# Kernel tuning notes

Hardware: AMD Instinct MI355X
Metric: run time of the kernel (lower is better)

The kernel has to match this reference:

```python
import jax, jax.numpy as jnp
import numpy as np

B, S, DIM = 1, 2048, 2048
H = 16
Q_LORA, KV_LORA = 1536, 512
D_NOPE, D_ROPE, D_V = 128, 64, 128
D_QK = D_NOPE + D_ROPE  # 192
EPS = 1e-6


def rms_norm(x, w, eps=EPS):
    var = jnp.mean(jnp.square(x), axis=-1, keepdims=True)
    return x * jax.lax.rsqrt(var + eps) * w


def apply_rope(x, cos, sin):
    # x: [B,S,H,D] with interleaved complex pairs; cos/sin: [S,D//2]
    x1, x2 = x[..., 0::2], x[..., 1::2]
    c = cos[None, :, None, :]
    s = sin[None, :, None, :]
    o1 = x1 * c - x2 * s
    o2 = x1 * s + x2 * c
    return jnp.stack([o1, o2], axis=-1).reshape(x.shape)


def setup_inputs() -> dict:
    key = jax.random.key(0)
    ks = jax.random.split(key, 8)
    x = jax.random.normal(ks[0], (B, S, DIM), dtype=jnp.float32)
    # rotary tables (standard complex exponentials)
    inv_freq = 1.0 / (10000.0 ** (np.arange(0, D_ROPE, 2, dtype=np.float32) / D_ROPE))
    t = np.arange(S, dtype=np.float32)
    freqs = np.outer(t, inv_freq)  # [S, D_ROPE//2]
    freqs_cos = jnp.asarray(np.cos(freqs))
    freqs_sin = jnp.asarray(np.sin(freqs))
    sd = lambda fan_in: 1.0 / np.sqrt(fan_in)
    wq_a = jax.random.normal(ks[1], (Q_LORA, DIM), dtype=jnp.float32) * sd(DIM)
    q_a_ln_w = jnp.ones((Q_LORA,), dtype=jnp.float32)
    wq_b = jax.random.normal(ks[2], (H * D_QK, Q_LORA), dtype=jnp.float32) * sd(Q_LORA)
    wkv_a = jax.random.normal(ks[3], (KV_LORA + D_ROPE, DIM), dtype=jnp.float32) * sd(DIM)
    kv_a_ln_w = jnp.ones((KV_LORA,), dtype=jnp.float32)
    wkv_b = jax.random.normal(ks[4], (H * (D_NOPE + D_V), KV_LORA), dtype=jnp.float32) * sd(KV_LORA)
    wo = jax.random.normal(ks[5], (DIM, H * D_V), dtype=jnp.float32) * sd(H * D_V)
    return {"x": x, "freqs_cos": freqs_cos, "freqs_sin": freqs_sin,
            "wq_a": wq_a, "q_a_ln_w": q_a_ln_w, "wq_b": wq_b,
            "wkv_a": wkv_a, "kv_a_ln_w": kv_a_ln_w, "wkv_b": wkv_b, "wo": wo}


def reference(x, freqs_cos, freqs_sin, wq_a, q_a_ln_w, wq_b, wkv_a, kv_a_ln_w, wkv_b, wo):
    softmax_scale = D_QK ** -0.5
    # Query: low-rank down-proj -> RMSNorm -> up-proj
    q = rms_norm(x @ wq_a.T, q_a_ln_w) @ wq_b.T            # [B,S,H*D_QK]
    q = q.reshape(B, S, H, D_QK)
    q_nope, q_pe = q[..., :D_NOPE], q[..., D_NOPE:]
    q_pe = apply_rope(q_pe, freqs_cos, freqs_sin)
    # KV: shared low-rank latent + decoupled rope key (MQA-style, 1 head)
    kv = x @ wkv_a.T                                        # [B,S,KV_LORA+D_ROPE]
    kv_c = rms_norm(kv[..., :KV_LORA], kv_a_ln_w)           # [B,S,KV_LORA]
    k_pe = apply_rope(kv[..., None, KV_LORA:], freqs_cos, freqs_sin)  # [B,S,1,D_ROPE]
    kvb = (kv_c @ wkv_b.T).reshape(B, S, H, D_NOPE + D_V)
    k_nope, v = kvb[..., :D_NOPE], kvb[..., D_NOPE:]
    # Attention scores: nope part + shared rope part
    scores = (jnp.einsum('bqhd,bkhd->bhqk', q_nope, k_nope)
              + jnp.einsum('bqhd,bkd->bhqk', q_pe, k_pe[:, :, 0, :])) * softmax_scale
    causal = jnp.tril(jnp.ones((S, S), dtype=bool))
    scores = jnp.where(causal[None, None], scores, -jnp.inf)
    p = jax.nn.softmax(scores, axis=-1)
    out = jnp.einsum('bhqk,bkhd->bqhd', p, v).reshape(B, S, H * D_V)
    return out @ wo.T
```

## Files before the change

### kernel.cpp

```cpp
#include <hip/hip_runtime.h>
#include <cstdint>
#include <cstddef>

typedef __bf16 bf16;
typedef bf16 bf16x8 __attribute__((ext_vector_type(8)));
typedef bf16 bf16x4 __attribute__((ext_vector_type(4)));
typedef float f32x4 __attribute__((ext_vector_type(4)));

typedef __attribute__((address_space(1))) void as1_void;
typedef __attribute__((address_space(3))) void as3_void;

#define INF __builtin_inff()

__global__ __launch_bounds__(256) void z100_cast_all(
    const float* __restrict__ x, const float* __restrict__ wq_a,
    const float* __restrict__ wkv_a, const float* __restrict__ wq_b,
    const float* __restrict__ wkv_b, const float* __restrict__ wo,
    bf16* __restrict__ x_bf, bf16* __restrict__ wab_bf,
    bf16* __restrict__ wqb_bf, bf16* __restrict__ wkvb_bf,
    bf16* __restrict__ wo_bf) {
    int i = blockIdx.x * 256 + threadIdx.x;
    const float* s;
    bf16* d;
    float mul = 1.f;
    if (i < 1048576)      { s = x + (size_t)i * 4;                     d = x_bf + (size_t)i * 4; }
    else if (i < 1835008) { int o = i - 1048576; s = wq_a  + (size_t)o * 4; d = wab_bf + (size_t)o * 4; }
    else if (i < 2129920) { int o = i - 1835008; s = wkv_a + (size_t)o * 4; d = wab_bf + 1536ull * 2048 + (size_t)o * 4; }
    else if (i < 3309568) { int o = i - 2129920; s = wq_b  + (size_t)o * 4; d = wqb_bf + (size_t)o * 4;
                            mul = 0.072168783649f; }
    else if (i < 3833856) { int o = i - 3309568; s = wkv_b + (size_t)o * 4; d = wkvb_bf + (size_t)o * 4; }
    else if (i < 4882432) { int o = i - 3833856; s = wo    + (size_t)o * 4; d = wo_bf + (size_t)o * 4; }
    else {                  int o = i - 4882432; bf16x4 z = {};
                            *(bf16x4*)(wab_bf + 2112ull * 2048 + (size_t)o * 4) = z; return; }
    float4 v = *(const float4*)s;
    bf16x4 ovec = { (bf16)(v.x * mul), (bf16)(v.y * mul), (bf16)(v.z * mul), (bf16)(v.w * mul) };
    *(bf16x4*)d = ovec;
}

__global__ __launch_bounds__(256) void z100_rmsnorm2(
    const bf16* __restrict__ qa, const float* __restrict__ q_ln,
    const float* __restrict__ kv_ln,
    bf16* __restrict__ qan, bf16* __restrict__ kvc) {
    const int bid = blockIdx.x;
    const bf16* xr;
    const float* w;
    bf16* yr;
    int N; float invN;
    if (bid < 2048) { xr = qa + (size_t)bid * 2112;        w = q_ln;  yr = qan + (size_t)bid * 1536; N = 1536; invN = 1.f / 1536.f; }
    else { int r = bid - 2048; xr = qa + (size_t)r * 2112 + 1536; w = kv_ln; yr = kvc + (size_t)r * 512;  N = 512;  invN = 1.f / 512.f; }
    float ss = 0.f;
    for (int i = threadIdx.x * 8; i < N; i += 2048) {
        bf16x8 v = *(const bf16x8*)(xr + i);
        #pragma unroll
        for (int j = 0; j < 8; ++j) { float f = (float)v[j]; ss += f * f; }
    }
    #pragma unroll
    for (int d = 1; d < 64; d <<= 1) ss += __shfl_xor(ss, d);
    __shared__ float red[4];
    if ((threadIdx.x & 63) == 0) red[threadIdx.x >> 6] = ss;
    __syncthreads();
    float tot = red[0] + red[1] + red[2] + red[3];
    float rs = rsqrtf(tot * invN + 1e-6f);
    for (int i = threadIdx.x * 8; i < N; i += 2048) {
        bf16x8 v = *(const bf16x8*)(xr + i);
        float4 w0 = *(const float4*)(w + i);
        float4 w1 = *(const float4*)(w + i + 4);
        bf16x8 o;
        o[0] = (bf16)((float)v[0] * rs * w0.x); o[1] = (bf16)((float)v[1] * rs * w0.y);
        o[2] = (bf16)((float)v[2] * rs * w0.z); o[3] = (bf16)((float)v[3] * rs * w0.w);
        o[4] = (bf16)((float)v[4] * rs * w1.x); o[5] = (bf16)((float)v[5] * rs * w1.y);
        o[6] = (bf16)((float)v[6] * rs * w1.z); o[7] = (bf16)((float)v[7] * rs * w1.w);
        *(bf16x8*)(yr + i) = o;
    }
}

template <typename OutT>
__device__ __forceinline__ void gemm8_body(
    const bf16* __restrict__ A, const bf16* __restrict__ B,
    OutT* __restrict__ C, int N, int K, int ldc, int mblk, int nblk,
    bf16* AsB, bf16* BsB) {
    const int tid = threadIdx.x;
    const int lane = tid & 63, wave = tid >> 6;
    const int l15 = lane & 15, l4 = lane >> 4;
    const int m0 = mblk * 128, n0 = nblk * 128;
    const int wr = (wave >> 1) * 32, wc = (wave & 1) * 64;

    f32x4 acc[2][4] = {};

    const int srow = lane >> 2;
    const int scol = (lane & 3) * 8;
    const size_t a_base = (size_t)(m0 + wave * 16 + srow) * K + scol;
    const size_t b_base = (size_t)(n0 + wave * 16 + srow) * K + scol;

    auto stg = [&](int buf, int k0) {
        __builtin_amdgcn_global_load_lds((as1_void*)(void*)(A + a_base + k0),
                                         (as3_void*)(AsB + buf * 4096 + wave * 512), 16, 0, 0);
        __builtin_amdgcn_global_load_lds((as1_void*)(void*)(B + b_base + k0),
                                         (as3_void*)(BsB + buf * 4096 + wave * 512), 16, 0, 0);
    };

    const int nt = K >> 5;
    stg(0, 0);
    stg(1, 32);
    asm volatile("s_waitcnt vmcnt(2)" ::: "memory");
    __builtin_amdgcn_s_barrier();

    int cb = 0, sb = 2;
    for (int t = 0; t < nt; ++t) {
        if (t + 2 < nt) stg(sb, (t + 2) * 32);
        const bf16* Ab = AsB + cb * 4096;
        const bf16* Bb = BsB + cb * 4096;
        bf16x8 fa[2], fb[4];
        #pragma unroll
        for (int i = 0; i < 2; ++i)
            fa[i] = *(const bf16x8*)(Ab + (wr + 16 * i + l15) * 32 + 8 * l4);
        #pragma unroll
        for (int j = 0; j < 4; ++j)
            fb[j] = *(const bf16x8*)(Bb + (wc + 16 * j + l15) * 32 + 8 * l4);
        #pragma unroll
        for (int i = 0; i < 2; ++i)
            #pragma unroll
            for (int j = 0; j < 4; ++j)
                acc[i][j] = __builtin_amdgcn_mfma_f32_16x16x32_bf16(fa[i], fb[j], acc[i][j], 0, 0, 0);
        if (t + 2 < nt) { asm volatile("s_waitcnt vmcnt(2)" ::: "memory"); }
        else            { asm volatile("s_waitcnt vmcnt(0)" ::: "memory"); }
        __builtin_amdgcn_s_barrier();
        cb = (cb == 2) ? 0 : cb + 1;
        sb = (sb == 2) ? 0 : sb + 1;
    }

    #pragma unroll
    for (int i = 0; i < 2; ++i) {
        int row0 = m0 + wr + 16 * i + 4 * l4;
        #pragma unroll
        for (int j = 0; j < 4; ++j) {
            int col = n0 + wc + 16 * j + l15;
            if (col < N) {
                #pragma unroll
                for (int jj = 0; jj < 4; ++jj)
                    C[(size_t)(row0 + jj) * ldc + col] = (OutT)acc[i][j][jj];
            }
        }
    }
}

__global__ __launch_bounds__(512) void z100_gemm8(
    const bf16* __restrict__ A, const bf16* __restrict__ B,
    float* __restrict__ C, int N, int K, int ldc) {
    __shared__ alignas(16) bf16 As[3 * 128 * 32];
    __shared__ alignas(16) bf16 Bs[3 * 128 * 32];
    gemm8_body<float>(A, B, C, N, K, ldc, blockIdx.y, blockIdx.x, As, Bs);
}

__global__ __launch_bounds__(512) void z100_gemm8_bf(
    const bf16* __restrict__ A, const bf16* __restrict__ B,
    bf16* __restrict__ C, int N, int K, int ldc) {
    __shared__ alignas(16) bf16 As[3 * 128 * 32];
    __shared__ alignas(16) bf16 Bs[3 * 128 * 32];
    gemm8_body<bf16>(A, B, C, N, K, ldc, blockIdx.y, blockIdx.x, As, Bs);
}

__global__ __launch_bounds__(512) void z100_gemm_qkv(
    const bf16* __restrict__ qan, const bf16* __restrict__ wqb, bf16* __restrict__ qf,
    const bf16* __restrict__ kvc, const bf16* __restrict__ wkvb, bf16* __restrict__ kvbf) {
    __shared__ alignas(16) bf16 As[3 * 128 * 32];
    __shared__ alignas(16) bf16 Bs[3 * 128 * 32];
    const int bid = blockIdx.x;
    if (bid < 384) gemm8_body<bf16>(qan, wqb, qf, 3072, 1536, 3072, bid / 24, bid % 24, As, Bs);
    else { int b = bid - 384; gemm8_body<bf16>(kvc, wkvb, kvbf, 4096, 512, 4096, b / 32, b % 32, As, Bs); }
}

__global__ __launch_bounds__(256) void z100_prep(
    const bf16* __restrict__ kvb, const bf16* __restrict__ q_f,
    const bf16* __restrict__ qa,
    const float* __restrict__ fc, const float* __restrict__ fs,
    bf16* __restrict__ vt, bf16* __restrict__ qpe, bf16* __restrict__ kpe) {
    const int bid = blockIdx.x;
    const int tid = threadIdx.x;
    if (bid < 512) {
        const int st = bid & 31, h = bid >> 5;
        const int s0 = st * 64;
        __shared__ alignas(16) bf16 tile[64 * 132];
        #pragma unroll
        for (int i = 0; i < 4; ++i) {
            int slot = i * 256 + tid;
            int r = slot >> 4, c8 = slot & 15;
            bf16x8 v = *(const bf16x8*)(kvb + (size_t)(s0 + r) * 4096 + h * 256 + 128 + c8 * 8);
            *(bf16x8*)(tile + r * 132 + c8 * 8) = v;
        }
        __syncthreads();
        #pragma unroll
        for (int i = 0; i < 4; ++i) {
            int slot = i * 256 + tid;
            int d = slot >> 3, ch = slot & 7;
            bf16x8 o;
            #pragma unroll
            for (int j = 0; j < 8; ++j) o[j] = tile[(ch * 8 + j) * 132 + d];
            *(bf16x8*)(vt + ((size_t)h * 128 + d) * 2048 + s0 + ch * 8) = o;
        }
        return;
    }
    const int QTOT = 2048 * 16 * 32;
    int u = (bid - 512) * 256 + tid;
    if (u < QTOT) {
        int i = u & 31;
        int h = (u >> 5) & 15;
        int s = u >> 9;
        float c = fc[s * 32 + i], sn = fs[s * 32 + i];
        float x1 = (float)q_f[(size_t)s * 3072 + h * 192 + 128 + 2 * i];
        float x2 = (float)q_f[(size_t)s * 3072 + h * 192 + 128 + 2 * i + 1];
        qpe[(size_t)s * 1024 + h * 64 + 2 * i]     = (bf16)(x1 * c - x2 * sn);
        qpe[(size_t)s * 1024 + h * 64 + 2 * i + 1] = (bf16)(x1 * sn + x2 * c);
    } else {
        int v = u - QTOT;
        int i = v & 31;
        int s = v >> 5;
        float c = fc[s * 32 + i], sn = fs[s * 32 + i];
        float x1 = (float)qa[(size_t)s * 2112 + 2048 + 2 * i];
        float x2 = (float)qa[(size_t)s * 2112 + 2048 + 2 * i + 1];
        kpe[(size_t)s * 64 + 2 * i]     = (bf16)(x1 * c - x2 * sn);
        kpe[(size_t)s * 64 + 2 * i + 1] = (bf16)(x1 * sn + x2 * c);
    }
}

__global__ __launch_bounds__(512) void z100_attn(
    const bf16* __restrict__ q_f, const bf16* __restrict__ qpe,
    const bf16* __restrict__ kvb, const bf16* __restrict__ kpe,
    const bf16* __restrict__ v_t, bf16* __restrict__ opart, float* __restrict__ ml) {
    const int bid = blockIdx.x;
    const int wk = (bid & 7) * 80 + (bid >> 3);
    const int h = wk / 40;
    const int s0w = wk - h * 40;
    int qt = 0, rem = s0w;
    while (rem >= (qt >> 2) + 1) { rem -= (qt >> 2) + 1; ++qt; }
    const int chk = rem;
    const int q0 = qt * 128;
    const int kstart = chk * 512;
    const int kend = min(q0 + 128, kstart + 512);
    const int slot = h * 40 + s0w;

    const int tid = threadIdx.x;
    const int lane = tid & 63, wave = tid >> 6;
    const int l15 = lane & 15, l4 = lane >> 4;

    __shared__ alignas(16) bf16 Ks[2][64 * 192];
    __shared__ alignas(16) bf16 Vs[2][128 * 64];

    const bf16* Vh = v_t + (size_t)h * 128 * 2048;

    const int wrow_max = q0 + wave * 16 + 15;
    const int diag_k0 = q0 + (wave >> 2) * 64;

    bf16x8 qf[6];
    {
        const int qrow = q0 + wave * 16 + l15;
        const bf16* qn = q_f + (size_t)qrow * 3072 + h * 192 + 8 * l4;
        #pragma unroll
        for (int c = 0; c < 4; ++c) qf[c] = *(const bf16x8*)(qn + 32 * c);
        const bf16* qp = qpe + (size_t)qrow * 1024 + h * 64 + 8 * l4;
        qf[4] = *(const bf16x8*)(qp);
        qf[5] = *(const bf16x8*)(qp + 32);
    }

    const bf16* kp0[3];
    int kstep[3];
    #pragma unroll
    for (int i = 0; i < 3; ++i) {
        int off = (wave * 3 + i) * 1024 + lane * 16;
        int r = off / 384;
        int ch = (off % 384) >> 4;
        int ksrc = (r & 0x23) | ((r & 0x0C) << 1) | ((r & 0x10) >> 2);
        int chx = ch ^ (r & 7);
        if (chx < 16) { kp0[i] = kvb + (size_t)ksrc * 4096 + h * 256 + chx * 8; kstep[i] = 4096; }
        else          { kp0[i] = kpe + (size_t)ksrc * 64 + (chx - 16) * 8;      kstep[i] = 64; }
    }
    int voff[2];
    #pragma unroll
    for (int i = 0; i < 2; ++i) {
        int off = (wave * 2 + i) * 1024 + lane * 16;
        int d = off >> 7;
        int ch = (off >> 4) & 7;
        voff[i] = d * 2048 + (ch ^ (d & 7)) * 8;
    }

    auto stage = [&](int buf, int k0) {
        #pragma unroll
        for (int i = 0; i < 3; ++i)
            __builtin_amdgcn_global_load_lds(
                (as1_void*)(void*)(kp0[i] + (size_t)k0 * kstep[i]),
                (as3_void*)((char*)&Ks[buf][0] + (wave * 3 + i) * 1024), 16, 0, 0);
        #pragma unroll
        for (int i = 0; i < 2; ++i)
            __builtin_amdgcn_global_load_lds(
                (as1_void*)(void*)(Vh + k0 + voff[i]),
                (as3_void*)((char*)&Vs[buf][0] + (wave * 2 + i) * 1024), 16, 0, 0);
    };

    f32x4 oacc[8] = {};
    float m_r = -INF, l_r = 0.f;
    const int nt = (kend - kstart) >> 6;

    stage(0, kstart);
    __syncthreads();
    int cur = 0;
    for (int t = 0; t < nt; ++t) {
        const int k0 = kstart + t * 64;
        if (t + 1 < nt) stage(cur ^ 1, k0 + 64);

        if (k0 <= wrow_max) {
            const char* KsC = (const char*)&Ks[cur][0];
            const char* VsC = (const char*)&Vs[cur][0];

            f32x4 sc[4];
            __builtin_amdgcn_s_setprio(1);
            #pragma unroll
            for (int kt = 0; kt < 4; ++kt) {
                f32x4 a = { 0.f, 0.f, 0.f, 0.f };
                int r = 16 * kt + l15;
                #pragma unroll
                for (int c = 0; c < 6; ++c) {
                    int byteo = (r * 384 + c * 64 + l4 * 16) ^ ((r & 7) << 4);
                    bf16x8 kf = *(const bf16x8*)(KsC + byteo);
                    a = __builtin_amdgcn_mfma_f32_16x16x32_bf16(kf, qf[c], a, 0, 0, 0);
                }
                sc[kt] = a;
            }
            __builtin_amdgcn_s_setprio(0);

            if (k0 == diag_k0) {
                int qrow = (wave & 3) * 16 + l15;
                #pragma unroll
                for (int kt = 0; kt < 4; ++kt)
                    #pragma unroll
                    for (int r = 0; r < 4; ++r) {
                        int kl = ((kt >> 1) << 5) | (l4 << 3) | ((kt & 1) << 2) | r;
                        if (kl > qrow) sc[kt][r] = -INF;
                    }
            }

            float mx = -INF;
            #pragma unroll
            for (int kt = 0; kt < 4; ++kt)
                #pragma unroll
                for (int r = 0; r < 4; ++r) mx = fmaxf(mx, sc[kt][r]);
            mx = fmaxf(mx, __shfl_xor(mx, 16));
            mx = fmaxf(mx, __shfl_xor(mx, 32));
            if (!__all(mx <= m_r + 8.f)) {
                float mnew = fmaxf(m_r, mx);
                float corr = __expf(m_r - mnew);
                float c_r[4];
                #pragma unroll
                for (int r = 0; r < 4; ++r) c_r[r] = __shfl(corr, 20 * l4 + r);
                #pragma unroll
                for (int dt = 0; dt < 8; ++dt)
                    #pragma unroll
                    for (int r = 0; r < 4; ++r) oacc[dt][r] *= c_r[r];
                l_r *= corr;
                m_r = mnew;
            }
            float rs = 0.f;
            #pragma unroll
            for (int kt = 0; kt < 4; ++kt)
                #pragma unroll
                for (int r = 0; r < 4; ++r) {
                    float pv = __expf(sc[kt][r] - m_r);
                    sc[kt][r] = pv;
                    rs += pv;
                }
            rs += __shfl_xor(rs, 16);
            rs += __shfl_xor(rs, 32);
            l_r += rs;

            bf16x8 pf[2];
            #pragma unroll
            for (int c2 = 0; c2 < 2; ++c2)
                #pragma unroll
                for (int i = 0; i < 8; ++i)
                    pf[c2][i] = (bf16)sc[2 * c2 + (i >> 2)][i & 3];

            __builtin_amdgcn_s_setprio(1);
            #pragma unroll
            for (int dt = 0; dt < 8; ++dt) {
                #pragma unroll
                for (int c2 = 0; c2 < 2; ++c2) {
                    int d = 16 * dt + l15;
                    int byteo = (d * 128 + c2 * 64 + l4 * 16) ^ ((d & 7) << 4);
                    bf16x8 vf = *(const bf16x8*)(VsC + byteo);
                    oacc[dt] = __builtin_amdgcn_mfma_f32_16x16x32_bf16(pf[c2], vf, oacc[dt], 0, 0, 0);
                }
            }
            __builtin_amdgcn_s_setprio(0);
        }

        __syncthreads();
        cur ^= 1;
    }

    const int qr_base = wave * 16;
    if (lane < 16) {
        ml[(size_t)slot * 256 + qr_base + lane] = m_r;
        ml[(size_t)slot * 256 + 128 + qr_base + lane] = l_r;
    }
    bf16* ob = opart + (size_t)slot * 16384;
    #pragma unroll
    for (int dt = 0; dt < 8; ++dt) {
        int d = 16 * dt + l15;
        #pragma unroll
        for (int r = 0; r < 4; ++r) {
            int qr = qr_base + 4 * l4 + r;
            ob[qr * 128 + d] = (bf16)oacc[dt][r];
        }
    }
}

__global__ __launch_bounds__(512) void z100_attn_combine(
    const bf16* __restrict__ opart, const float* __restrict__ ml, bf16* __restrict__ ao) {
    const int qt = blockIdx.x, h = blockIdx.y;
    const int t = threadIdx.x;
    const int np = (qt >> 2) + 1;
    int base = 0;
    for (int j = 0; j < qt; ++j) base += (j >> 2) + 1;
    const int slot0 = h * 40 + base;
    #pragma unroll 1
    for (int it = 0; it < 4; ++it) {
        const int c = it * 512 + t;
        const int qr = c >> 4;
        const int dc = (c & 15) * 8;
        float m[4], l[4], w[4];
        float M = -INF;
        #pragma unroll
        for (int i = 0; i < 4; ++i)
            if (i < np) {
                m[i] = ml[(size_t)(slot0 + i) * 256 + qr];
                l[i] = ml[(size_t)(slot0 + i) * 256 + 128 + qr];
                M = fmaxf(M, m[i]);
            }
        float L = 0.f;
        #pragma unroll
        for (int i = 0; i < 4; ++i)
            if (i < np) {
                w[i] = __expf(m[i] - M);
                L += w[i] * l[i];
            }
        float invL = 1.f / L;
        float acc[8] = {};
        #pragma unroll
        for (int i = 0; i < 4; ++i)
            if (i < np) {
                bf16x8 a = *(const bf16x8*)(opart + (size_t)(slot0 + i) * 16384 + (size_t)c * 8);
                #pragma unroll
                for (int j = 0; j < 8; ++j) acc[j] += w[i] * (float)a[j];
            }
        bf16x8 o;
        #pragma unroll
        for (int j = 0; j < 8; ++j) o[j] = (bf16)(acc[j] * invL);
        *(bf16x8*)(ao + (size_t)(qt * 128 + qr) * 2048 + h * 128 + dc) = o;
    }
}

extern "C" void kernel_launch(void* const* d_in, const int* in_sizes, int n_in,
                              void* d_out, int out_size, void* d_ws, size_t ws_size,
                              hipStream_t stream) {
    (void)in_sizes; (void)n_in; (void)out_size; (void)ws_size;
    const float* x     = (const float*)d_in[0];
    const float* fc    = (const float*)d_in[1];
    const float* fs    = (const float*)d_in[2];
    const float* wq_a  = (const float*)d_in[3];
    const float* q_ln  = (const float*)d_in[4];
    const float* wq_b  = (const float*)d_in[5];
    const float* wkv_a = (const float*)d_in[6];
    const float* kv_ln = (const float*)d_in[7];
    const float* wkv_b = (const float*)d_in[8];
    const float* wo    = (const float*)d_in[9];
    float* out = (float*)d_out;

    char* p = (char*)d_ws;
    auto alloc = [&](size_t bytes) {
        char* r = p;
        p += (bytes + 255) & ~(size_t)255;
        return r;
    };
    char* phase1  = p;
    bf16* x_bf    = (bf16*)alloc(2048ull * 2048 * 2);
    bf16* wab_bf  = (bf16*)alloc(2176ull * 2048 * 2);
    bf16* qa_bf   = (bf16*)alloc(2048ull * 2112 * 2);
    bf16* qan_bf  = (bf16*)alloc(2048ull * 1536 * 2);
    bf16* wqb_bf  = (bf16*)alloc(3072ull * 1536 * 2);
    bf16* wkvb_bf = (bf16*)alloc(4096ull * 512 * 2);
    bf16* wo_bf   = (bf16*)alloc(2048ull * 2048 * 2);
    bf16* q_f     = (bf16*)alloc(2048ull * 3072 * 2);
    bf16* kvc_bf  = (bf16*)alloc(2048ull * 512 * 2);
    bf16* kvb_f   = (bf16*)alloc(2048ull * 4096 * 2);
    bf16* qpe     = (bf16*)alloc(2048ull * 16 * 64 * 2);
    bf16* kpe     = (bf16*)alloc(2048ull * 64 * 2);
    bf16* v_t     = (bf16*)alloc(16ull * 128 * 2048 * 2);
    bf16* ao_bf   = (bf16*)alloc(2048ull * 2048 * 2);
    bf16* opart   = (bf16*)phase1;
    float* mlbuf  = (float*)(phase1 + 640ull * 16384 * 2);

    z100_cast_all<<<19200, 256, 0, stream>>>(x, wq_a, wkv_a, wq_b, wkv_b, wo,
                                             x_bf, wab_bf, wqb_bf, wkvb_bf, wo_bf);

    z100_gemm8_bf<<<dim3(17, 16), 512, 0, stream>>>(x_bf, wab_bf, qa_bf, 2112, 2048, 2112);
    z100_rmsnorm2<<<4096, 256, 0, stream>>>(qa_bf, q_ln, kv_ln, qan_bf, kvc_bf);

    z100_gemm_qkv<<<dim3(896), 512, 0, stream>>>(qan_bf, wqb_bf, q_f, kvc_bf, wkvb_bf, kvb_f);

    z100_prep<<<4864, 256, 0, stream>>>(kvb_f, q_f, qa_bf, fc, fs, v_t, qpe, kpe);

    z100_attn<<<dim3(640), 512, 0, stream>>>(q_f, qpe, kvb_f, kpe, v_t, opart, mlbuf);
    z100_attn_combine<<<dim3(16, 16), 512, 0, stream>>>(opart, mlbuf, ao_bf);

    z100_gemm8<<<dim3(16, 16), 512, 0, stream>>>(ao_bf, wo_bf, out, 2048, 2048, 2048);
}
```

Baseline: 218.9 us.

## Process two query row groups per wave in attention to reuse K fragments

The attention kernel now covers 256 query rows per block, with each wave holding two 16-row query groups. Every K fragment loaded from LDS feeds two MFMAs, which raises compute per LDS read. The split-K work is re-tiled into 256-key chunks (36 slots per head), and the combine kernel is adjusted to match. The lazy rescale skip is dropped, so each step now always applies the softmax correction. The doubled accumulators raise register pressure, and rows that are fully masked issue MFMAs on zero probabilities.

```diff
diff --git a/kernel.cpp b/kernel.cpp
--- a/kernel.cpp
+++ b/kernel.cpp
@@ -228,16 +228,15 @@
     const bf16* __restrict__ kvb, const bf16* __restrict__ kpe,
     const bf16* __restrict__ v_t, bf16* __restrict__ opart, float* __restrict__ ml) {
     const int bid = blockIdx.x;
-    const int wk = (bid & 7) * 80 + (bid >> 3);
-    const int h = wk / 40;
-    const int s0w = wk - h * 40;
+    const int wk = (bid & 7) * 72 + (bid >> 3);
+    const int h = wk / 36;
+    const int s0w = wk - h * 36;
     int qt = 0, rem = s0w;
-    while (rem >= (qt >> 2) + 1) { rem -= (qt >> 2) + 1; ++qt; }
+    while (rem >= qt + 1) { rem -= qt + 1; ++qt; }
     const int chk = rem;
-    const int q0 = qt * 128;
-    const int kstart = chk * 512;
-    const int kend = min(q0 + 128, kstart + 512);
-    const int slot = h * 40 + s0w;
+    const int q0 = qt * 256;
+    const int kstart = chk * 256;
+    const int slot = h * 36 + s0w;
 
     const int tid = threadIdx.x;
     const int lane = tid & 63, wave = tid >> 6;
@@ -247,19 +246,18 @@
     __shared__ alignas(16) bf16 Vs[2][128 * 64];
 
     const bf16* Vh = v_t + (size_t)h * 128 * 2048;
-
-    const int wrow_max = q0 + wave * 16 + 15;
-    const int diag_k0 = q0 + (wave >> 2) * 64;
-
-    bf16x8 qf[6];
-    {
-        const int qrow = q0 + wave * 16 + l15;
+    const int wq0 = q0 + wave * 32;
+
+    bf16x8 qf[2][6];
+    #pragma unroll
+    for (int g = 0; g < 2; ++g) {
+        const int qrow = wq0 + g * 16 + l15;
         const bf16* qn = q_f + (size_t)qrow * 3072 + h * 192 + 8 * l4;
         #pragma unroll
-        for (int c = 0; c < 4; ++c) qf[c] = *(const bf16x8*)(qn + 32 * c);
+        for (int c = 0; c < 4; ++c) qf[g][c] = *(const bf16x8*)(qn + 32 * c);
         const bf16* qp = qpe + (size_t)qrow * 1024 + h * 64 + 8 * l4;
-        qf[4] = *(const bf16x8*)(qp);
-        qf[5] = *(const bf16x8*)(qp + 32);
+        qf[g][4] = *(const bf16x8*)(qp);
+        qf[g][5] = *(const bf16x8*)(qp + 32);
     }
 
     const bf16* kp0[3];
@@ -296,87 +294,105 @@
                 (as3_void*)((char*)&Vs[buf][0] + (wave * 2 + i) * 1024), 16, 0, 0);
     };
 
-    f32x4 oacc[8] = {};
-    float m_r = -INF, l_r = 0.f;
-    const int nt = (kend - kstart) >> 6;
+    f32x4 oacc0[8] = {}, oacc1[8] = {};
+    float m_r0 = -INF, m_r1 = -INF, l_r0 = 0.f, l_r1 = 0.f;
+
+    auto softmax_g = [&](float& mr, float& lr, f32x4 (&oac)[8],
+                         f32x4 (&scg)[4], bf16x8 (&pfg)[2]) {
+        float mx = -INF;
+        #pragma unroll
+        for (int kt = 0; kt < 4; ++kt)
+            #pragma unroll
+            for (int r = 0; r < 4; ++r) mx = fmaxf(mx, scg[kt][r]);
+        mx = fmaxf(mx, __shfl_xor(mx, 16));
+        mx = fmaxf(mx, __shfl_xor(mx, 32));
+        float mnew = fmaxf(mr, mx);
+        float corr = __expf(mr - mnew);
+        float rs = 0.f;
+        #pragma unroll
+        for (int kt = 0; kt < 4; ++kt)
+            #pragma unroll
+            for (int r = 0; r < 4; ++r) {
+                float pv = __expf(scg[kt][r] - mnew);
+                scg[kt][r] = pv;
+                rs += pv;
+            }
+        rs += __shfl_xor(rs, 16);
+        rs += __shfl_xor(rs, 32);
+        lr = lr * corr + rs;
+        mr = mnew;
+        float c_r[4];
+        #pragma unroll
+        for (int r = 0; r < 4; ++r) c_r[r] = __shfl(corr, 20 * l4 + r);
+        #pragma unroll
+        for (int dt = 0; dt < 8; ++dt)
+            #pragma unroll
+            for (int r = 0; r < 4; ++r) oac[dt][r] *= c_r[r];
+        #pragma unroll
+        for (int c2 = 0; c2 < 2; ++c2)
+            #pragma unroll
+            for (int i = 0; i < 8; ++i)
+                pfg[c2][i] = (bf16)scg[2 * c2 + (i >> 2)][i & 3];
+    };
 
     stage(0, kstart);
     __syncthreads();
     int cur = 0;
-    for (int t = 0; t < nt; ++t) {
+    #pragma unroll 1
+    for (int t = 0; t < 4; ++t) {
         const int k0 = kstart + t * 64;
-        if (t + 1 < nt) stage(cur ^ 1, k0 + 64);
-
-        if (k0 <= wrow_max) {
+        if (t + 1 < 4) stage(cur ^ 1, k0 + 64);
+
+        const bool act1 = (k0 <= wq0 + 31);
+        const bool act0 = (k0 <= wq0 + 15);
+        if (act1) {
             const char* KsC = (const char*)&Ks[cur][0];
             const char* VsC = (const char*)&Vs[cur][0];
 
-            f32x4 sc[4];
+            f32x4 sc[2][4];
             __builtin_amdgcn_s_setprio(1);
             #pragma unroll
             for (int kt = 0; kt < 4; ++kt) {
-                f32x4 a = { 0.f, 0.f, 0.f, 0.f };
+                f32x4 a0 = { 0.f, 0.f, 0.f, 0.f };
+                f32x4 a1 = { 0.f, 0.f, 0.f, 0.f };
                 int r = 16 * kt + l15;
                 #pragma unroll
                 for (int c = 0; c < 6; ++c) {
                     int byteo = (r * 384 + c * 64 + l4 * 16) ^ ((r & 7) << 4);
                     bf16x8 kf = *(const bf16x8*)(KsC + byteo);
-                    a = __builtin_amdgcn_mfma_f32_16x16x32_bf16(kf, qf[c], a, 0, 0, 0);
+                    a0 = __builtin_amdgcn_mfma_f32_16x16x32_bf16(kf, qf[0][c], a0, 0, 0, 0);
+                    a1 = __builtin_amdgcn_mfma_f32_16x16x32_bf16(kf, qf[1][c], a1, 0, 0, 0);
                 }
-                sc[kt] = a;
+                sc[0][kt] = a0;
+                sc[1][kt] = a1;
             }
             __builtin_amdgcn_s_setprio(0);
 
-            if (k0 == diag_k0) {
-                int qrow = (wave & 3) * 16 + l15;
+            #pragma unroll
+            for (int g = 0; g < 2; ++g) {
+                int gidx = (wave << 1) + g;
+                if (k0 == q0 + (gidx >> 2) * 64) {
+                    int qrow = (gidx & 3) * 16 + l15;
+                    #pragma unroll
+                    for (int kt = 0; kt < 4; ++kt)
+                        #pragma unroll
+                        for (int r = 0; r < 4; ++r) {
+                            int kl = ((kt >> 1) << 5) | (l4 << 3) | ((kt & 1) << 2) | r;
+                            if (kl > qrow) sc[g][kt][r] = -INF;
+                        }
+                }
+            }
+
+            bf16x8 pf0[2], pf1[2];
+            softmax_g(m_r1, l_r1, oacc1, sc[1], pf1);
+            if (act0) {
+                softmax_g(m_r0, l_r0, oacc0, sc[0], pf0);
+            } else {
                 #pragma unroll
-                for (int kt = 0; kt < 4; ++kt)
+                for (int c2 = 0; c2 < 2; ++c2)
                     #pragma unroll
-                    for (int r = 0; r < 4; ++r) {
-                        int kl = ((kt >> 1) << 5) | (l4 << 3) | ((kt & 1) << 2) | r;
-                        if (kl > qrow) sc[kt][r] = -INF;
-                    }
-            }
-
-            float mx = -INF;
-            #pragma unroll
-            for (int kt = 0; kt < 4; ++kt)
-                #pragma unroll
-                for (int r = 0; r < 4; ++r) mx = fmaxf(mx, sc[kt][r]);
-            mx = fmaxf(mx, __shfl_xor(mx, 16));
-            mx = fmaxf(mx, __shfl_xor(mx, 32));
-            if (!__all(mx <= m_r + 8.f)) {
-                float mnew = fmaxf(m_r, mx);
-                float corr = __expf(m_r - mnew);
-                float c_r[4];
-                #pragma unroll
-                for (int r = 0; r < 4; ++r) c_r[r] = __shfl(corr, 20 * l4 + r);
-                #pragma unroll
-                for (int dt = 0; dt < 8; ++dt)
-                    #pragma unroll
-                    for (int r = 0; r < 4; ++r) oacc[dt][r] *= c_r[r];
-                l_r *= corr;
-                m_r = mnew;
-            }
-            float rs = 0.f;
-            #pragma unroll
-            for (int kt = 0; kt < 4; ++kt)
-                #pragma unroll
-                for (int r = 0; r < 4; ++r) {
-                    float pv = __expf(sc[kt][r] - m_r);
-                    sc[kt][r] = pv;
-                    rs += pv;
-                }
-            rs += __shfl_xor(rs, 16);
-            rs += __shfl_xor(rs, 32);
-            l_r += rs;
-
-            bf16x8 pf[2];
-            #pragma unroll
-            for (int c2 = 0; c2 < 2; ++c2)
-                #pragma unroll
-                for (int i = 0; i < 8; ++i)
-                    pf[c2][i] = (bf16)sc[2 * c2 + (i >> 2)][i & 3];
+                    for (int i = 0; i < 8; ++i) pf0[c2][i] = (bf16)0.f;
+            }
 
             __builtin_amdgcn_s_setprio(1);
             #pragma unroll
@@ -386,7 +402,8 @@
                     int d = 16 * dt + l15;
                     int byteo = (d * 128 + c2 * 64 + l4 * 16) ^ ((d & 7) << 4);
                     bf16x8 vf = *(const bf16x8*)(VsC + byteo);
-                    oacc[dt] = __builtin_amdgcn_mfma_f32_16x16x32_bf16(pf[c2], vf, oacc[dt], 0, 0, 0);
+                    oacc1[dt] = __builtin_amdgcn_mfma_f32_16x16x32_bf16(pf1[c2], vf, oacc1[dt], 0, 0, 0);
+                    oacc0[dt] = __builtin_amdgcn_mfma_f32_16x16x32_bf16(pf0[c2], vf, oacc0[dt], 0, 0, 0);
                 }
             }
             __builtin_amdgcn_s_setprio(0);
@@ -396,19 +413,21 @@
         cur ^= 1;
     }
 
-    const int qr_base = wave * 16;
     if (lane < 16) {
-        ml[(size_t)slot * 256 + qr_base + lane] = m_r;
-        ml[(size_t)slot * 256 + 128 + qr_base + lane] = l_r;
-    }
-    bf16* ob = opart + (size_t)slot * 16384;
+        ml[(size_t)slot * 512 + wave * 32 + lane] = m_r0;
+        ml[(size_t)slot * 512 + wave * 32 + 16 + lane] = m_r1;
+        ml[(size_t)slot * 512 + 256 + wave * 32 + lane] = l_r0;
+        ml[(size_t)slot * 512 + 256 + wave * 32 + 16 + lane] = l_r1;
+    }
+    bf16* ob = opart + (size_t)slot * 32768;
     #pragma unroll
     for (int dt = 0; dt < 8; ++dt) {
         int d = 16 * dt + l15;
         #pragma unroll
         for (int r = 0; r < 4; ++r) {
-            int qr = qr_base + 4 * l4 + r;
-            ob[qr * 128 + d] = (bf16)oacc[dt][r];
+            int qr0 = wave * 32 + 4 * l4 + r;
+            ob[qr0 * 128 + d] = (bf16)oacc0[dt][r];
+            ob[(qr0 + 16) * 128 + d] = (bf16)oacc1[dt][r];
         }
     }
 }
@@ -417,27 +436,26 @@
     const bf16* __restrict__ opart, const float* __restrict__ ml, bf16* __restrict__ ao) {
     const int qt = blockIdx.x, h = blockIdx.y;
     const int t = threadIdx.x;
-    const int np = (qt >> 2) + 1;
-    int base = 0;
-    for (int j = 0; j < qt; ++j) base += (j >> 2) + 1;
-    const int slot0 = h * 40 + base;
+    const int np = qt + 1;
+    const int base = qt * (qt + 1) / 2;
+    const int slot0 = h * 36 + base;
     #pragma unroll 1
-    for (int it = 0; it < 4; ++it) {
+    for (int it = 0; it < 8; ++it) {
         const int c = it * 512 + t;
         const int qr = c >> 4;
         const int dc = (c & 15) * 8;
-        float m[4], l[4], w[4];
+        float m[8], l[8], w[8];
         float M = -INF;
         #pragma unroll
-        for (int i = 0; i < 4; ++i)
+        for (int i = 0; i < 8; ++i)
             if (i < np) {
-                m[i] = ml[(size_t)(slot0 + i) * 256 + qr];
-                l[i] = ml[(size_t)(slot0 + i) * 256 + 128 + qr];
+                m[i] = ml[(size_t)(slot0 + i) * 512 + qr];
+                l[i] = ml[(size_t)(slot0 + i) * 512 + 256 + qr];
                 M = fmaxf(M, m[i]);
             }
         float L = 0.f;
         #pragma unroll
-        for (int i = 0; i < 4; ++i)
+        for (int i = 0; i < 8; ++i)
             if (i < np) {
                 w[i] = __expf(m[i] - M);
                 L += w[i] * l[i];
@@ -445,16 +463,16 @@
         float invL = 1.f / L;
         float acc[8] = {};
         #pragma unroll
-        for (int i = 0; i < 4; ++i)
+        for (int i = 0; i < 8; ++i)
             if (i < np) {
-                bf16x8 a = *(const bf16x8*)(opart + (size_t)(slot0 + i) * 16384 + (size_t)c * 8);
+                bf16x8 a = *(const bf16x8*)(opart + (size_t)(slot0 + i) * 32768 + (size_t)c * 8);
                 #pragma unroll
                 for (int j = 0; j < 8; ++j) acc[j] += w[i] * (float)a[j];
             }
         bf16x8 o;
         #pragma unroll
         for (int j = 0; j < 8; ++j) o[j] = (bf16)(acc[j] * invL);
-        *(bf16x8*)(ao + (size_t)(qt * 128 + qr) * 2048 + h * 128 + dc) = o;
+        *(bf16x8*)(ao + (size_t)(qt * 256 + qr) * 2048 + h * 128 + dc) = o;
     }
 }
 
@@ -496,7 +514,7 @@
     bf16* v_t     = (bf16*)alloc(16ull * 128 * 2048 * 2);
     bf16* ao_bf   = (bf16*)alloc(2048ull * 2048 * 2);
     bf16* opart   = (bf16*)phase1;
-    float* mlbuf  = (float*)(phase1 + 640ull * 16384 * 2);
+    float* mlbuf  = (float*)(phase1 + 576ull * 32768 * 2);
 
     z100_cast_all<<<19200, 256, 0, stream>>>(x, wq_a, wkv_a, wq_b, wkv_b, wo,
                                              x_bf, wab_bf, wqb_bf, wkvb_bf, wo_bf);
@@ -508,8 +526,8 @@
 
     z100_prep<<<4864, 256, 0, stream>>>(kvb_f, q_f, qa_bf, fc, fs, v_t, qpe, kpe);
 
-    z100_attn<<<dim3(640), 512, 0, stream>>>(q_f, qpe, kvb_f, kpe, v_t, opart, mlbuf);
-    z100_attn_combine<<<dim3(16, 16), 512, 0, stream>>>(opart, mlbuf, ao_bf);
+    z100_attn<<<dim3(576), 512, 0, stream>>>(q_f, qpe, kvb_f, kpe, v_t, opart, mlbuf);
+    z100_attn_combine<<<dim3(8, 16), 512, 0, stream>>>(opart, mlbuf, ao_bf);
 
     z100_gemm8<<<dim3(16, 16), 512, 0, stream>>>(ao_bf, wo_bf, out, 2048, 2048, 2048);
 }
```

Result: slower. 243.2 us (+11.1%).
